# Performance work log

Measured on AMD Instinct MI355X. Metric: run time of the kernel, lower is better.

Reference implementation:

```python
import jax, jax.numpy as jnp
import numpy as np

EPS = 1e-5


def conv2d(x, w, b, pad, mode='reflect'):
    # x: [B,C,H,W], w: [O,I,kh,kw]
    if pad > 0:
        x = jnp.pad(x, ((0, 0), (0, 0), (pad, pad), (pad, pad)), mode=mode)
    y = jax.lax.conv_general_dilated(x, w, (1, 1), 'VALID',
                                     dimension_numbers=('NCHW', 'OIHW', 'NCHW'))
    return y + b[None, :, None, None]


def inorm(x):
    # InstanceNorm2d, no affine (nn.InstanceNorm2d default)
    m = jnp.mean(x, axis=(2, 3), keepdims=True)
    v = jnp.mean((x - m) ** 2, axis=(2, 3), keepdims=True)
    return (x - m) * jax.lax.rsqrt(v + EPS)


def upsample2(x):
    # nn.Upsample(scale_factor=2), default nearest
    return jnp.repeat(jnp.repeat(x, 2, axis=2), 2, axis=3)


def bilinear_sample(img, py, px):
    # img [B,C,H,W]; py/px [B,H,W] float coords; zero padding outside bounds
    B, C, H, W = img.shape
    y0 = jnp.floor(py)
    x0 = jnp.floor(px)
    wy1 = (py - y0)[:, None]
    wx1 = (px - x0)[:, None]
    wy0 = 1.0 - wy1
    wx0 = 1.0 - wx1
    y0i = y0.astype(jnp.int32)
    x0i = x0.astype(jnp.int32)
    flat = img.reshape(B, C, H * W)

    def tap(yi, xi):
        valid = (yi >= 0) & (yi < H) & (xi >= 0) & (xi < W)
        idx = jnp.clip(yi, 0, H - 1) * W + jnp.clip(xi, 0, W - 1)
        g = jnp.take_along_axis(flat, idx.reshape(B, 1, H * W), axis=2).reshape(B, C, H, W)
        return g * valid[:, None]

    return (tap(y0i, x0i) * wy0 * wx0 + tap(y0i, x0i + 1) * wy0 * wx1 +
            tap(y0i + 1, x0i) * wy1 * wx0 + tap(y0i + 1, x0i + 1) * wy1 * wx1)


def mdcn(x, offset, mask, w, b):
    # modulated deformable conv v2: 3x3, stride 1, pad 1, 1 deformable group
    # offset [B,18,H,W] read as interleaved (dy,dx) per kernel tap; mask [B,9,H,W]
    B, C, H, W = x.shape
    off = offset.reshape(B, 9, 2, H, W)
    base_y = jnp.arange(H, dtype=x.dtype)[None, :, None]
    base_x = jnp.arange(W, dtype=x.dtype)[None, None, :]
    cols = []
    for k in range(9):
        ky, kx = k // 3 - 1, k % 3 - 1
        py = base_y + ky + off[:, k, 0]
        px = base_x + kx + off[:, k, 1]
        cols.append(bilinear_sample(x, py, px) * mask[:, k][:, None])
    col = jnp.stack(cols, axis=2)  # [B,C,9,H,W]
    out = jnp.einsum('bckhw,ock->bohw', col, w.reshape(w.shape[0], C, 9))
    return out + b[None, :, None, None]


def dcn_block(out, skip, off_w, off_b, w, b):
    # ModulatedDeformConvPack(double=True): offsets from concat, deform conv on skip
    dc = jnp.concatenate([out, skip], axis=1)
    om = conv2d(dc, off_w, off_b, 1, mode='constant')
    o1, o2, m = jnp.split(om, 3, axis=1)
    offset = jnp.concatenate([o1, o2], axis=1)
    pre = mdcn(skip, offset, jax.nn.sigmoid(m), w, b)
    return jnp.concatenate([pre, out], axis=1), offset


def decoder_fwd(x, skip1, skip2,
                rb0_w1, rb0_b1, rb0_w2, rb0_b2,
                rb1_w1, rb1_b1, rb1_w2, rb1_b2,
                conv1_w, conv1_b, conv3_w, conv3_b,
                conv5_w, conv5_b, conv6_w, conv6_b,
                dcn2_off_w, dcn2_off_b, dcn2_w, dcn2_b,
                dcn1_off_w, dcn1_off_b, dcn1_w, dcn1_b):
    out = x
    # i=0: ResBlocks (2 resblocks, 'in' norm, relu, reflect pad)
    for (w1, b1, w2, b2) in ((rb0_w1, rb0_b1, rb0_w2, rb0_b2),
                             (rb1_w1, rb1_b1, rb1_w2, rb1_b2)):
        h = jax.nn.relu(inorm(conv2d(out, w1, b1, 1)))
        out = out + inorm(conv2d(h, w2, b2, 1))
    # i=1: Conv2dBlock(256->256, 5x5)
    out = jax.nn.relu(inorm(conv2d(out, conv1_w, conv1_b, 2)))
    # dcn_2 hook (baseline_idx=2 -> dcn_idx=[1,3])
    out, offset2 = dcn_block(out, skip2, dcn2_off_w, dcn2_off_b, dcn2_w, dcn2_b)
    # i=2: upsample
    out = upsample2(out)
    # i=3: Conv2dBlock(512->128, 5x5)
    out = jax.nn.relu(inorm(conv2d(out, conv3_w, conv3_b, 2)))
    # dcn hook
    out, offset1 = dcn_block(out, skip1, dcn1_off_w, dcn1_off_b, dcn1_w, dcn1_b)
    # i=4: upsample
    out = upsample2(out)
    # i=5: Conv2dBlock(256->64, 5x5)
    out = jax.nn.relu(inorm(conv2d(out, conv5_w, conv5_b, 2)))
    # i=6: Conv2dBlock(64->3, 7x7, no norm, tanh)
    out = jnp.tanh(conv2d(out, conv6_w, conv6_b, 3))
    offset_sum = 0.5 * (jnp.mean(jnp.abs(offset1)) + jnp.mean(jnp.abs(offset2)))
    return out, offset_sum


def setup_inputs() -> dict:
    key = jax.random.key(0)
    ks = iter(jax.random.split(key, 48))

    def randn(shape, scale=1.0):
        return jax.random.normal(next(ks), shape, dtype=jnp.float32) * scale

    def conv_w(o, i, k, scale=1.0):
        return randn((o, i, k, k), scale / float(np.sqrt(i * k * k)))

    d = {}
    d['x'] = randn((8, 256, 32, 32))
    d['skip1'] = randn((8, 128, 64, 64))
    d['skip2'] = randn((8, 256, 32, 32))
    for r in range(2):
        d[f'rb{r}_w1'] = conv_w(256, 256, 3)
        d[f'rb{r}_b1'] = randn((256,), 0.01)
        d[f'rb{r}_w2'] = conv_w(256, 256, 3)
        d[f'rb{r}_b2'] = randn((256,), 0.01)
    d['conv1_w'] = conv_w(256, 256, 5); d['conv1_b'] = randn((256,), 0.01)
    d['conv3_w'] = conv_w(128, 512, 5); d['conv3_b'] = randn((128,), 0.01)
    d['conv5_w'] = conv_w(64, 256, 5); d['conv5_b'] = randn((64,), 0.01)
    d['conv6_w'] = conv_w(3, 64, 7); d['conv6_b'] = randn((3,), 0.01)
    d['dcn2_off_w'] = conv_w(27, 512, 3, 0.1); d['dcn2_off_b'] = randn((27,), 0.01)
    d['dcn2_w'] = conv_w(256, 256, 3); d['dcn2_b'] = randn((256,), 0.01)
    d['dcn1_off_w'] = conv_w(27, 256, 3, 0.1); d['dcn1_off_b'] = randn((27,), 0.01)
    d['dcn1_w'] = conv_w(128, 128, 3); d['dcn1_b'] = randn((128,), 0.01)
    return d


def reference(x, skip1, skip2,
              rb0_w1, rb0_b1, rb0_w2, rb0_b2,
              rb1_w1, rb1_b1, rb1_w2, rb1_b2,
              conv1_w, conv1_b, conv3_w, conv3_b,
              conv5_w, conv5_b, conv6_w, conv6_b,
              dcn2_off_w, dcn2_off_b, dcn2_w, dcn2_b,
              dcn1_off_w, dcn1_off_b, dcn1_w, dcn1_b):
    return decoder_fwd(x, skip1, skip2,
                       rb0_w1, rb0_b1, rb0_w2, rb0_b2,
                       rb1_w1, rb1_b1, rb1_w2, rb1_b2,
                       conv1_w, conv1_b, conv3_w, conv3_b,
                       conv5_w, conv5_b, conv6_w, conv6_b,
                       dcn2_off_w, dcn2_off_b, dcn2_w, dcn2_b,
                       dcn1_off_w, dcn1_off_b, dcn1_w, dcn1_b)
```

## Files before the change

kernel.cpp:

```cpp
#include <hip/hip_runtime.h>
#include <hip/hip_bf16.h>
#include <math.h>

typedef __hip_bfloat16 bf16;
typedef unsigned short u16;
typedef __attribute__((ext_vector_type(8))) short short8;
typedef __attribute__((ext_vector_type(4))) float f32x4;

__device__ __forceinline__ float LD(const float* p) { return *p; }
__device__ __forceinline__ float LD(const bf16* p)  { return __bfloat162float(*p); }
__device__ __forceinline__ void  ST(float* p, float v) { *p = v; }
__device__ __forceinline__ void  ST(bf16* p, float v)  { *p = __float2bfloat16(v); }
__device__ __forceinline__ u16   f2b(float v) { bf16 h = __float2bfloat16(v); return *reinterpret_cast<u16*>(&h); }
__device__ __forceinline__ float b2fu(u16 u) { bf16 h = *reinterpret_cast<bf16*>(&u); return __bfloat162float(h); }

__global__ __launch_bounds__(256) void copy_kernel(const float* __restrict__ in,
                                                   float* __restrict__ out, int n) {
    int i = blockIdx.x * blockDim.x + threadIdx.x;
    if (i < n) out[i] = in[i];
}

__global__ __launch_bounds__(256) void nhwc_split_kernel(const float* __restrict__ in,
                                                         u16* __restrict__ hi, u16* __restrict__ lo,
                                                         int C, int HW)
{
    __shared__ float tile[32][65];
    const int b = blockIdx.z;
    const int c0 = blockIdx.y * 32;
    const int p0 = blockIdx.x * 64;
    for (int i = threadIdx.x; i < 2048; i += 256) {
        const int c_ = i >> 6, p_ = i & 63;
        tile[c_][p_] = in[((size_t)(b * C + c0 + c_)) * HW + p0 + p_];
    }
    __syncthreads();
    for (int i = threadIdx.x; i < 2048; i += 256) {
        const int p_ = i >> 5, c_ = i & 31;
        const float v = tile[c_][p_];
        const bf16 h = __float2bfloat16(v);
        const float hv = __bfloat162float(h);
        const bf16 l = __float2bfloat16(v - hv);
        const size_t dst = ((size_t)b * HW + p0 + p_) * C + c0 + c_;
        hi[dst] = *(const u16*)&h;
        lo[dst] = *(const u16*)&l;
    }
}

__global__ __launch_bounds__(256) void wsplit_kernel(const float* __restrict__ w,
                                                     u16* __restrict__ hi, u16* __restrict__ lo,
                                                     int O, int C, int KK)
{
    const int i = blockIdx.x * 256 + threadIdx.x;
    const int n = O * C * KK;
    if (i >= n) return;
    const int o = i / (C * KK);
    const int r = i - o * C * KK;
    const int c = r / KK;
    const int t = r - c * KK;
    const float v = w[i];
    const bf16 h = __float2bfloat16(v);
    const float hv = __bfloat162float(h);
    const bf16 l = __float2bfloat16(v - hv);
    const size_t dst = ((size_t)t * O + o) * C + c;
    hi[dst] = *(const u16*)&h;
    lo[dst] = *(const u16*)&l;
}

__global__ __launch_bounds__(256) void wsplit2_kernel(const float* __restrict__ w,
                                                      u16* __restrict__ hi, u16* __restrict__ lo,
                                                      int O, int C, int KK)
{
    const int i = blockIdx.x * 256 + threadIdx.x;
    const int n = O * C * KK;
    if (i >= n) return;
    const int o = i / (C * KK);
    const int r = i - o * C * KK;
    const int c = r / KK;
    const int t = r - c * KK;
    const float v = w[i];
    const bf16 h = __float2bfloat16(v);
    const float hv = __bfloat162float(h);
    const bf16 l = __float2bfloat16(v - hv);
    const int nch = C >> 5;
    const int cc = c >> 5, quad = (c >> 3) & 3, q = c & 7;
    const size_t dst = ((((size_t)t * nch + cc) * 4 + quad) * O + o) * 8 + q;
    hi[dst] = *(const u16*)&h;
    lo[dst] = *(const u16*)&l;
}

__global__ __launch_bounds__(256) void wsplitL_kernel(const float* __restrict__ w,
        u16* __restrict__ lh, u16* __restrict__ ll, u16* __restrict__ ch, int O, int C)
{
    const int i = blockIdx.x * 256 + threadIdx.x;
    const int n = O * C * 50;
    if (i >= n) return;
    const int s = i / (O * C);
    const int r = i - s * (O * C);
    const int o = r / C;
    const int c = r - o * C;
    const size_t U = (size_t)C * O;
    const int cc = c >> 5, quad = (c >> 3) & 3, q = c & 7;
    const size_t din = (((size_t)cc * 4 + quad) * O + o) * 8 + q;
    const float* wp = w + ((size_t)o * C + c) * 25;
    if (s < 30) {
        const int ry = s / 15, rem = s % 15, j = rem / 5, tx = rem % 5;
        int ys, yn;
        if (ry == 0) { ys = (j == 0) ? 0 : (j == 1) ? 2 : 4; yn = (j == 2) ? 1 : 2; }
        else         { ys = (j == 0) ? 0 : (j == 1) ? 1 : 3; yn = (j == 0) ? 1 : 2; }
        float v = 0.f;
        for (int ty = ys; ty < ys + yn; ++ty) v += wp[ty * 5 + tx];
        const bf16 h = __float2bfloat16(v);
        const bf16 l = __float2bfloat16(v - __bfloat162float(h));
        lh[(size_t)s * U + din] = *(const u16*)&h;
        ll[(size_t)s * U + din] = *(const u16*)&l;
    } else {
        const int t = s - 30;
        const int cidx = t / 5, tx = t - cidx * 5;
        const int tyc = (cidx == 0) ? 0 : (cidx == 1) ? 1 : (cidx == 2) ? 3 : 4;
        const bf16 h = __float2bfloat16(wp[tyc * 5 + tx]);
        ch[(size_t)t * U + din] = *(const u16*)&h;
    }
}

template<typename T1, typename T2, int K, bool UP, int EPI, bool ASPLIT,
         int NR, int NCOL, int MT, int MW>
__global__ __launch_bounds__(MW * 128) void conv_mfma3(
        const T1* __restrict__ src1, const T2* __restrict__ src2,
        int C1, int C,
        const u16* __restrict__ wth, const u16* __restrict__ wtl,
        const float* __restrict__ bias,
        void* __restrict__ outv, int O, int H, int W)
{
    constexpr int KK = K * K;
    constexpr int ATILE = NR * NCOL * 32;
    __shared__ __align__(16) u16 Ah[ATILE];
    __shared__ __align__(16) u16 Al[ASPLIT ? ATILE : 8];

    const int tid  = threadIdx.x;
    const int lane = tid & 63;
    const int wv   = tid >> 6;
    const int ln15 = lane & 15;
    const int quad = lane >> 4;
    const int mi = wv % MW, ni = wv / MW;
    const int b = blockIdx.y;
    const int p0 = blockIdx.x * (MT * 16 * MW);
    const int obase = blockIdx.z * 64;
    const int HW = H * W;
    const int SH = UP ? (H >> 1) : H;
    const int SW = UP ? (W >> 1) : W;
    const int SHW = SH * SW;
    const int PAD = K / 2;
    const int C2 = C - C1;
    const int nch = C >> 5;

    const int y0 = p0 / W;
    const int rbase = (y0 <= PAD) ? 0 : (UP ? ((y0 - PAD) >> 1) : (y0 - PAD));

    int rs[MT][K], cs[MT][K];
#pragma unroll
    for (int ms = 0; ms < MT; ++ms) {
        const int pm = p0 + mi * (MT * 16) + ms * 16 + ln15;
        const int ym = pm / W, xm = pm - ym * W;
#pragma unroll
        for (int tt = 0; tt < K; ++tt) {
            int yy = ym + tt - PAD;
            yy = yy < 0 ? -yy : yy; yy = yy >= H ? 2 * H - 2 - yy : yy;
            rs[ms][tt] = (UP ? (yy >> 1) : yy) - rbase;
            int xx = xm + tt - PAD;
            xx = xx < 0 ? -xx : xx; xx = xx >= W ? 2 * W - 2 - xx : xx;
            cs[ms][tt] = UP ? (xx >> 1) : xx;
        }
    }

    f32x4 acc[MT][2];
#pragma unroll
    for (int i = 0; i < MT; ++i)
#pragma unroll
        for (int j = 0; j < 2; ++j) acc[i][j] = (f32x4)0.f;

    for (int cc = 0; cc < nch; ++cc) {
        const int c0 = cc << 5;
        __syncthreads();
        for (int idx = tid; idx < NR * NCOL * 4; idx += MW * 128) {
            const int c_ = idx % NCOL;
            const int r_ = (idx / NCOL) % NR;
            const int cq = idx / (NCOL * NR);
            int rr = rbase + r_; rr = rr >= SH ? SH - 1 : rr;
            const int sidx = rr * SW + c_;
            short8 vh, vl;
#pragma unroll
            for (int q = 0; q < 8; ++q) {
                const int c = c0 + cq * 8 + q;
                float v;
                if (c < C1) v = LD(src1 + (size_t)(b * C1 + c) * SHW + sidx);
                else        v = LD(src2 + (size_t)(b * C2 + (c - C1)) * SHW + sidx);
                const u16 hv = f2b(v);
                vh[q] = (short)hv;
                if (ASPLIT) vl[q] = (short)f2b(v - b2fu(hv));
            }
            *(short8*)&Ah[idx * 8] = vh;
            if (ASPLIT) *(short8*)&Al[idx * 8] = vl;
        }
        __syncthreads();

#pragma unroll
        for (int t = 0; t < KK; ++t) {
            const int ty = t / K, tx = t - ty * K;
            const size_t wb0 = ((((size_t)t * nch + cc) * 4 + quad) * O
                                + obase + ni * 32 + ln15) * 8;
            const short8 b0h = *(const short8*)(wth + wb0);
            const short8 b1h = *(const short8*)(wth + wb0 + 128);
            const short8 b0l = *(const short8*)(wtl + wb0);
            const short8 b1l = *(const short8*)(wtl + wb0 + 128);
#pragma unroll
            for (int ms = 0; ms < MT; ++ms) {
                const int ao = ((quad * NR + rs[ms][ty]) * NCOL + cs[ms][tx]) * 8;
                const short8 a = *(const short8*)&Ah[ao];
                acc[ms][0] = __builtin_amdgcn_mfma_f32_16x16x32_bf16(a, b0h, acc[ms][0], 0, 0, 0);
                acc[ms][0] = __builtin_amdgcn_mfma_f32_16x16x32_bf16(a, b0l, acc[ms][0], 0, 0, 0);
                acc[ms][1] = __builtin_amdgcn_mfma_f32_16x16x32_bf16(a, b1h, acc[ms][1], 0, 0, 0);
                acc[ms][1] = __builtin_amdgcn_mfma_f32_16x16x32_bf16(a, b1l, acc[ms][1], 0, 0, 0);
                if (ASPLIT) {
                    const short8 al = *(const short8*)&Al[ao];
                    acc[ms][0] = __builtin_amdgcn_mfma_f32_16x16x32_bf16(al, b0h, acc[ms][0], 0, 0, 0);
                    acc[ms][1] = __builtin_amdgcn_mfma_f32_16x16x32_bf16(al, b1h, acc[ms][1], 0, 0, 0);
                }
            }
        }
    }

#pragma unroll
    for (int ms = 0; ms < MT; ++ms) {
#pragma unroll
        for (int ns = 0; ns < 2; ++ns) {
            const int o = obase + ni * 32 + ns * 16 + ln15;
            const float bv = bias[o];
            const f32x4 av = acc[ms][ns];
#pragma unroll
            for (int r = 0; r < 4; ++r) {
                const int pp = p0 + mi * (MT * 16) + ms * 16 + (quad << 2) + r;
                const float v = av[r] + bv;
                const size_t oidx = ((size_t)(b * O + o)) * HW + pp;
                if (EPI == 0) ((float*)outv)[oidx] = v;
                else          ((bf16*)outv)[oidx] = __float2bfloat16(v);
            }
        }
    }
}

template<typename T1, typename T2, int NR, int NCOL, int MT, int MW>
__global__ __launch_bounds__(MW * 128) void conv_mfma5(
        const T1* __restrict__ src1, const T2* __restrict__ src2,
        int C1, int C,
        const u16* __restrict__ wLh, const u16* __restrict__ wLl,
        const u16* __restrict__ wCh,
        const float* __restrict__ bias,
        bf16* __restrict__ out, int O, int H, int W)
{
    constexpr int NRR = NR + 1;
    __shared__ __align__(16) u16 Ah[4 * NRR * NCOL * 8];

    const int tid  = threadIdx.x;
    const int lane = tid & 63;
    const int wv   = tid >> 6;
    const int ln15 = lane & 15;
    const int quad = lane >> 4;
    const int mi = wv % MW, ni = wv / MW;
    const int b = blockIdx.y;
    const int p0 = blockIdx.x * (MT * 16 * MW);
    const int obase = blockIdx.z * 64;
    const int HW = H * W;
    const int SH = H >> 1, SW = W >> 1;
    const int SHW = SH * SW;
    const int C2 = C - C1;
    const int nch = C >> 5;
    const size_t U = (size_t)C * O;

    const int y0 = p0 / W;
    const int rbase = (y0 <= 2) ? 0 : ((y0 - 2) >> 1);

    const int ym0 = (p0 + mi * (MT * 16)) / W;
    const int ry = ym0 & 1;
    const int uu = ym0 >> 1;
    int r0 = uu - 1, r2 = uu + 1;
    r0 = r0 < 0 ? 1 : r0;
    r2 = r2 >= SH ? SH - 2 : r2;
    const int rg0 = r0 - rbase, rg1 = uu - rbase, rg2 = r2 - rbase;

    const bool isTopW = (ym0 <= 1), isBotW = (ym0 >= H - 2);
    const bool isBorderW = isTopW || isBotW;
    int cidx = 0;
    if (isTopW) cidx = (ym0 == 0) ? 1 : 0;
    if (isBotW) cidx = (ym0 == H - 2) ? 3 : 2;
    const bool blkTop = (p0 == 0);
    const bool blkBot = (p0 + MW * MT * 16 == HW);
    const bool blkEdge = blkTop || blkBot;

    int cs[MT][5];
#pragma unroll
    for (int ms = 0; ms < MT; ++ms) {
        const int pm = p0 + mi * (MT * 16) + ms * 16 + ln15;
        const int xm = pm % W;
#pragma unroll
        for (int tt = 0; tt < 5; ++tt) {
            int xx = xm + tt - 2;
            xx = xx < 0 ? -xx : xx; xx = xx >= W ? 2 * W - 2 - xx : xx;
            cs[ms][tt] = xx >> 1;
        }
    }

    f32x4 acc[MT][2];
#pragma unroll
    for (int i = 0; i < MT; ++i)
#pragma unroll
        for (int j = 0; j < 2; ++j) acc[i][j] = (f32x4)0.f;

    for (int cc = 0; cc < nch; ++cc) {
        const int c0 = cc << 5;
        __syncthreads();
        for (int idx = tid; idx < NR * NCOL * 4; idx += MW * 128) {
            const int c_ = idx % NCOL;
            const int r_ = (idx / NCOL) % NR;
            const int cq = idx / (NCOL * NR);
            int rr = rbase + r_; rr = rr >= SH ? SH - 1 : rr;
            const int sidx = rr * SW + c_;
            short8 vh;
#pragma unroll
            for (int q = 0; q < 8; ++q) {
                const int c = c0 + cq * 8 + q;
                float v;
                if (c < C1) v = LD(src1 + (size_t)(b * C1 + c) * SHW + sidx);
                else        v = LD(src2 + (size_t)(b * C2 + (c - C1)) * SHW + sidx);
                vh[q] = (short)f2b(v);
            }
            *(short8*)&Ah[((cq * NRR + r_) * NCOL + c_) * 8] = vh;
        }
        if (blkEdge) {
            const int ra = blkTop ? 0 : SH - 1;
            const int rb2 = blkTop ? 1 : SH - 2;
            for (int idx = tid; idx < NCOL * 4; idx += MW * 128) {
                const int c_ = idx % NCOL;
                const int cq = idx / NCOL;
                short8 vh;
#pragma unroll
                for (int q = 0; q < 8; ++q) {
                    const int c = c0 + cq * 8 + q;
                    float va, vb;
                    if (c < C1) {
                        const size_t base = (size_t)(b * C1 + c) * SHW;
                        va = LD(src1 + base + ra * SW + c_);
                        vb = LD(src1 + base + rb2 * SW + c_);
                    } else {
                        const size_t base = (size_t)(b * C2 + (c - C1)) * SHW;
                        va = LD(src2 + base + ra * SW + c_);
                        vb = LD(src2 + base + rb2 * SW + c_);
                    }
                    vh[q] = (short)f2b(va - vb);
                }
                *(short8*)&Ah[((cq * NRR + NR) * NCOL + c_) * 8] = vh;
            }
        }
        __syncthreads();

        const size_t wq = ((size_t)(cc * 4 + quad) * O + obase + ni * 32 + ln15) * 8;
#pragma unroll
        for (int j = 0; j < 3; ++j) {
            const int rgj = (j == 0) ? rg0 : (j == 1) ? rg1 : rg2;
#pragma unroll
            for (int tx = 0; tx < 5; ++tx) {
                const size_t wb = (size_t)((ry * 3 + j) * 5 + tx) * U + wq;
                const short8 b0h = *(const short8*)(wLh + wb);
                const short8 b1h = *(const short8*)(wLh + wb + 128);
                const short8 b0l = *(const short8*)(wLl + wb);
                const short8 b1l = *(const short8*)(wLl + wb + 128);
#pragma unroll
                for (int ms = 0; ms < MT; ++ms) {
                    const int ao = ((quad * NRR + rgj) * NCOL + cs[ms][tx]) * 8;
                    const short8 a = *(const short8*)&Ah[ao];
                    acc[ms][0] = __builtin_amdgcn_mfma_f32_16x16x32_bf16(a, b0h, acc[ms][0], 0, 0, 0);
                    acc[ms][0] = __builtin_amdgcn_mfma_f32_16x16x32_bf16(a, b0l, acc[ms][0], 0, 0, 0);
                    acc[ms][1] = __builtin_amdgcn_mfma_f32_16x16x32_bf16(a, b1h, acc[ms][1], 0, 0, 0);
                    acc[ms][1] = __builtin_amdgcn_mfma_f32_16x16x32_bf16(a, b1l, acc[ms][1], 0, 0, 0);
                }
            }
        }
        if (isBorderW) {
#pragma unroll
            for (int tx = 0; tx < 5; ++tx) {
                const size_t wb = (size_t)(cidx * 5 + tx) * U + wq;
                const short8 b0 = *(const short8*)(wCh + wb);
                const short8 b1 = *(const short8*)(wCh + wb + 128);
#pragma unroll
                for (int ms = 0; ms < MT; ++ms) {
                    const int ao = ((quad * NRR + NR) * NCOL + cs[ms][tx]) * 8;
                    const short8 a = *(const short8*)&Ah[ao];
                    acc[ms][0] = __builtin_amdgcn_mfma_f32_16x16x32_bf16(a, b0, acc[ms][0], 0, 0, 0);
                    acc[ms][1] = __builtin_amdgcn_mfma_f32_16x16x32_bf16(a, b1, acc[ms][1], 0, 0, 0);
                }
            }
        }
    }

#pragma unroll
    for (int ms = 0; ms < MT; ++ms) {
#pragma unroll
        for (int ns = 0; ns < 2; ++ns) {
            const int o = obase + ni * 32 + ns * 16 + ln15;
            const float bv = bias[o];
            const f32x4 av = acc[ms][ns];
#pragma unroll
            for (int r = 0; r < 4; ++r) {
                const int pp = p0 + mi * (MT * 16) + ms * 16 + (quad << 2) + r;
                out[((size_t)(b * O + o)) * HW + pp] = __float2bfloat16(av[r] + bv);
            }
        }
    }
}

template<typename OT, bool ASPLIT>
__global__ __launch_bounds__(256) void mdcn_mfma(
        const u16* __restrict__ skiph, const u16* __restrict__ skipl,
        const float* __restrict__ om,
        const u16* __restrict__ wth, const u16* __restrict__ wtl,
        const float* __restrict__ bias,
        OT* __restrict__ out, int C, int O, int H, int W)
{
    __shared__ float tpy[576], tpxs[576], tms[576];
    __shared__ __align__(16) u16 Ah[2][2048];
    __shared__ __align__(16) u16 Al[ASPLIT ? 2 : 1][2048];
    __shared__ __align__(16) u16 Bs[2][2][2048];

    const int tid = threadIdx.x;
    const int lane = tid & 63;
    const int wv = tid >> 6;
    const int ln15 = lane & 15;
    const int quad = lane >> 4;
    const int mi = wv & 1, ni = wv >> 1;
    const int flat = blockIdx.x + gridDim.x * (blockIdx.y + 8 * blockIdx.z);
    const int b = flat & 7;
    const int rest = flat >> 3;
    const int p0 = (rest % gridDim.x) * 64;
    const int obase = (rest / gridDim.x) * 64;
    const int HW = H * W;
    const int nch = C >> 5;

    const float* omb = om + (size_t)b * 27 * HW;
    for (int i = tid; i < 576; i += 256) {
        const int k = i >> 6, px_ = i & 63;
        const int p = p0 + px_;
        const int y = p / W, x = p - y * W;
        const float dy = omb[(2 * k) * HW + p];
        const float dx = omb[(2 * k + 1) * HW + p];
        const float mk = 1.f / (1.f + expf(-omb[(18 + k) * HW + p]));
        float py = (float)(y + k / 3 - 1) + dy;
        float pxx = (float)(x + k % 3 - 1) + dx;
        py  = fminf(fmaxf(py, -2.f), (float)H + 1.f);
        pxx = fminf(fmaxf(pxx, -2.f), (float)W + 1.f);
        tpy[i] = py; tpxs[i] = pxx; tms[i] = mk;
    }
    __syncthreads();

    f32x4 acc[2][2];
#pragma unroll
    for (int i = 0; i < 2; ++i)
#pragma unroll
        for (int j = 0; j < 2; ++j) acc[i][j] = (f32x4)0.f;

    const u16* xbh = skiph + (size_t)b * HW * C;
    const u16* xbl = skipl + (size_t)b * HW * C;
    const int swA = (lane >> 1) & 3;
    const int awr = (lane * 4 + (wv ^ swA)) * 8;
    const int pix0 = mi * 32 + ln15;
    const int pix1 = pix0 + 16;
    const int ao0 = (pix0 * 4 + (quad ^ ((pix0 >> 1) & 3))) * 8;
    const int ao1 = (pix1 * 4 + (quad ^ ((pix1 >> 1) & 3))) * 8;
    const int bo0 = (quad * 64 + ni * 32 + ln15) * 8;
    const int bo1 = bo0 + 16 * 8;

    int chunk = 0;
    for (int cc = 0; cc < nch; ++cc) {
        const int cbase = (cc << 5) + (wv << 3);
        for (int k = 0; k < 9; ++k, ++chunk) {
            const int s = chunk & 1;
            const float py = tpy[k * 64 + lane], pxx = tpxs[k * 64 + lane], mk = tms[k * 64 + lane];
            const float y0f = floorf(py), x0f = floorf(pxx);
            const int y0 = (int)y0f, x0 = (int)x0f;
            const float wy1 = py - y0f, wx1 = pxx - x0f;
            const float wy0 = 1.f - wy1, wx0 = 1.f - wx1;
            const bool r0v = (y0 >= 0 && y0 < H), r1v = (y0 + 1 >= 0 && y0 + 1 < H);
            const bool c0v = (x0 >= 0 && x0 < W), c1v = (x0 + 1 >= 0 && x0 + 1 < W);
            const float w00 = (r0v && c0v) ? wy0 * wx0 * mk : 0.f;
            const float w01 = (r0v && c1v) ? wy0 * wx1 * mk : 0.f;
            const float w10 = (r1v && c0v) ? wy1 * wx0 * mk : 0.f;
            const float w11 = (r1v && c1v) ? wy1 * wx1 * mk : 0.f;
            const int i00 = (r0v ? y0 : 0) * W + (c0v ? x0 : 0);
            const int i01 = (r0v ? y0 : 0) * W + (c1v ? x0 + 1 : 0);
            const int i10 = (r1v ? y0 + 1 : 0) * W + (c0v ? x0 : 0);
            const int i11 = (r1v ? y0 + 1 : 0) * W + (c1v ? x0 + 1 : 0);
            {
                const short8 h00 = *(const short8*)(xbh + (size_t)i00 * C + cbase);
                const short8 h01 = *(const short8*)(xbh + (size_t)i01 * C + cbase);
                const short8 h10 = *(const short8*)(xbh + (size_t)i10 * C + cbase);
                const short8 h11 = *(const short8*)(xbh + (size_t)i11 * C + cbase);
                const short8 l00 = *(const short8*)(xbl + (size_t)i00 * C + cbase);
                const short8 l01 = *(const short8*)(xbl + (size_t)i01 * C + cbase);
                const short8 l10 = *(const short8*)(xbl + (size_t)i10 * C + cbase);
                const short8 l11 = *(const short8*)(xbl + (size_t)i11 * C + cbase);
                short8 vh, vl;
#pragma unroll
                for (int q = 0; q < 8; ++q) {
                    const float x00 = b2fu((u16)h00[q]) + b2fu((u16)l00[q]);
                    const float x01 = b2fu((u16)h01[q]) + b2fu((u16)l01[q]);
                    const float x10 = b2fu((u16)h10[q]) + b2fu((u16)l10[q]);
                    const float x11 = b2fu((u16)h11[q]) + b2fu((u16)l11[q]);
                    const float v = w00 * x00 + w01 * x01 + w10 * x10 + w11 * x11;
                    const u16 hv = f2b(v);
                    vh[q] = (short)hv;
                    if (ASPLIT) vl[q] = (short)f2b(v - b2fu(hv));
                }
                *(short8*)&Ah[s][awr] = vh;
                if (ASPLIT) *(short8*)&Al[s][awr] = vl;
            }
            {
                const size_t base = ((((size_t)k * nch + cc) * 4 + wv) * O + obase + lane) * 8;
                *(short8*)&Bs[s][0][tid * 8] = *(const short8*)(wth + base);
                *(short8*)&Bs[s][1][tid * 8] = *(const short8*)(wtl + base);
            }
            __syncthreads();
            const short8 a0 = *(const short8*)&Ah[s][ao0];
            const short8 a1 = *(const short8*)&Ah[s][ao1];
            const short8 b0h = *(const short8*)&Bs[s][0][bo0];
            const short8 b1h = *(const short8*)&Bs[s][0][bo1];
            const short8 b0l = *(const short8*)&Bs[s][1][bo0];
            const short8 b1l = *(const short8*)&Bs[s][1][bo1];
            acc[0][0] = __builtin_amdgcn_mfma_f32_16x16x32_bf16(a0, b0h, acc[0][0], 0, 0, 0);
            acc[0][0] = __builtin_amdgcn_mfma_f32_16x16x32_bf16(a0, b0l, acc[0][0], 0, 0, 0);
            acc[0][1] = __builtin_amdgcn_mfma_f32_16x16x32_bf16(a0, b1h, acc[0][1], 0, 0, 0);
            acc[0][1] = __builtin_amdgcn_mfma_f32_16x16x32_bf16(a0, b1l, acc[0][1], 0, 0, 0);
            acc[1][0] = __builtin_amdgcn_mfma_f32_16x16x32_bf16(a1, b0h, acc[1][0], 0, 0, 0);
            acc[1][0] = __builtin_amdgcn_mfma_f32_16x16x32_bf16(a1, b0l, acc[1][0], 0, 0, 0);
            acc[1][1] = __builtin_amdgcn_mfma_f32_16x16x32_bf16(a1, b1h, acc[1][1], 0, 0, 0);
            acc[1][1] = __builtin_amdgcn_mfma_f32_16x16x32_bf16(a1, b1l, acc[1][1], 0, 0, 0);
            if (ASPLIT) {
                const short8 a0l = *(const short8*)&Al[s][ao0];
                const short8 a1l = *(const short8*)&Al[s][ao1];
                acc[0][0] = __builtin_amdgcn_mfma_f32_16x16x32_bf16(a0l, b0h, acc[0][0], 0, 0, 0);
                acc[0][1] = __builtin_amdgcn_mfma_f32_16x16x32_bf16(a0l, b1h, acc[0][1], 0, 0, 0);
                acc[1][0] = __builtin_amdgcn_mfma_f32_16x16x32_bf16(a1l, b0h, acc[1][0], 0, 0, 0);
                acc[1][1] = __builtin_amdgcn_mfma_f32_16x16x32_bf16(a1l, b1h, acc[1][1], 0, 0, 0);
            }
        }
    }

#pragma unroll
    for (int ms = 0; ms < 2; ++ms) {
#pragma unroll
        for (int ns = 0; ns < 2; ++ns) {
            const int o = obase + ni * 32 + ns * 16 + ln15;
            const float bv = bias[o];
#pragma unroll
            for (int r = 0; r < 4; ++r) {
                const int pp = p0 + mi * 32 + ms * 16 + (quad << 2) + r;
                ST(out + ((size_t)(b * O + o)) * HW + pp, acc[ms][ns][r] + bv);
            }
        }
    }
}

template<typename T1, typename T2, int K, bool REFLECT, bool UP, int NTN, int EPI, bool ASPLIT>
__global__ __launch_bounds__(256) void conv_mfma(
        const T1* __restrict__ src1, const T2* __restrict__ src2,
        int C1, int C,
        const u16* __restrict__ wth, const u16* __restrict__ wtl,
        const float* __restrict__ bias,
        void* __restrict__ outv, int O, int H, int W)
{
    constexpr int KK = K * K;
    __shared__ __align__(16) u16 As[64 * 40];
    __shared__ __align__(16) u16 Alo[ASPLIT ? 64 * 40 : 8];
    __shared__ __align__(16) u16 Bh[NTN * 16 * 40];
    __shared__ __align__(16) u16 Bl[NTN * 16 * 40];

    const int tid  = threadIdx.x;
    const int wv   = tid >> 6;
    const int lane = tid & 63;
    const int ln15 = lane & 15;
    const int flat = blockIdx.x + gridDim.x * blockIdx.y;
    const int b    = flat & 7;
    const int p0   = (flat >> 3) * 64;
    const int obase = blockIdx.z * (NTN * 16);
    const int HW = H * W;
    const int Hs = UP ? (H >> 1) : H;
    const int Ws = UP ? (W >> 1) : W;
    const int HsWs = Hs * Ws;
    const int PAD = K / 2;
    const int C2 = C - C1;
    const int m_stage = tid & 63;

    const int p = p0 + m_stage;
    const int y = p / W, x = p - y * W;
    int off[KK];
    float msk[KK];
#pragma unroll
    for (int ty = 0; ty < K; ++ty) {
#pragma unroll
        for (int tx = 0; tx < K; ++tx) {
            int yy = y + ty - PAD, xx = x + tx - PAD;
            bool vv = true;
            if (REFLECT) {
                yy = yy < 0 ? -yy : yy; yy = yy >= H ? 2 * H - 2 - yy : yy;
                xx = xx < 0 ? -xx : xx; xx = xx >= W ? 2 * W - 2 - xx : xx;
            } else {
                vv = (yy >= 0 && yy < H && xx >= 0 && xx < W);
                yy = yy < 0 ? 0 : (yy >= H ? H - 1 : yy);
                xx = xx < 0 ? 0 : (xx >= W ? W - 1 : xx);
            }
            off[ty * K + tx] = (UP ? (yy >> 1) : yy) * Ws + (UP ? (xx >> 1) : xx);
            msk[ty * K + tx] = vv ? 1.f : 0.f;
        }
    }

    f32x4 acc[NTN];
#pragma unroll
    for (int nt = 0; nt < NTN; ++nt) acc[nt] = (f32x4)0.f;

    const int aswz = (m_stage >> 3) & 3;
    const int awr  = m_stage * 40 + ((wv ^ aswz) << 3);
    const int arow = wv * 16 + ln15;
    const int ard  = arow * 40 + (((lane >> 4) ^ ((arow >> 3) & 3)) << 3);

    const int nch = C >> 5;
    for (int cc = 0; cc < nch; ++cc) {
        const int c0 = cc << 5;
        for (int t = 0; t < KK; ++t) {
            const int offt = off[t];
            const float mskt = msk[t];
            __syncthreads();
            {
                short8 avh, avl;
#pragma unroll
                for (int q = 0; q < 8; ++q) {
                    const int c = c0 + (wv << 3) + q;
                    float v;
                    if (c < C1) v = LD(src1 + ((size_t)(b * C1 + c)) * HsWs + offt);
                    else        v = LD(src2 + ((size_t)(b * C2 + (c - C1))) * HsWs + offt);
                    if (!REFLECT) v *= mskt;
                    const u16 hv = f2b(v);
                    avh[q] = (short)hv;
                    if (ASPLIT) avl[q] = (short)f2b(v - b2fu(hv));
                }
                *(short8*)&As[awr] = avh;
                if (ASPLIT) *(short8*)&Alo[awr] = avl;
            }
            for (int i = tid; i < NTN * 16 * 4; i += 256) {
                const int row = i >> 2, part = i & 3;
                int o = obase + row; if (o >= O) o = O - 1;
                const int pw = row * 40 + ((part ^ ((row >> 3) & 3)) << 3);
                const size_t wb = ((size_t)t * O + o) * C + c0 + (part << 3);
                *(short8*)&Bh[pw] = *(const short8*)(wth + wb);
                *(short8*)&Bl[pw] = *(const short8*)(wtl + wb);
            }
            __syncthreads();
            const short8 a = *(const short8*)&As[ard];
            short8 al;
            if (ASPLIT) al = *(const short8*)&Alo[ard];
#pragma unroll
            for (int nt = 0; nt < NTN; ++nt) {
                const int brow = nt * 16 + ln15;
                const int brd = brow * 40 + (((lane >> 4) ^ ((brow >> 3) & 3)) << 3);
                const short8 bh = *(const short8*)&Bh[brd];
                acc[nt] = __builtin_amdgcn_mfma_f32_16x16x32_bf16(a, bh, acc[nt], 0, 0, 0);
                const short8 bl = *(const short8*)&Bl[brd];
                acc[nt] = __builtin_amdgcn_mfma_f32_16x16x32_bf16(a, bl, acc[nt], 0, 0, 0);
                if (ASPLIT)
                    acc[nt] = __builtin_amdgcn_mfma_f32_16x16x32_bf16(al, bh, acc[nt], 0, 0, 0);
            }
        }
    }

#pragma unroll
    for (int nt = 0; nt < NTN; ++nt) {
        const int o = obase + nt * 16 + ln15;
        if (o < O) {
            const float bv = bias[o];
#pragma unroll
            for (int r = 0; r < 4; ++r) {
                const int pp = p0 + wv * 16 + ((lane >> 4) << 2) + r;
                const float v = acc[nt][r] + bv;
                const size_t oidx = ((size_t)(b * O + o)) * HW + pp;
                if (EPI == 0)      ((float*)outv)[oidx] = v;
                else if (EPI == 1) ((float*)outv)[oidx] = tanhf(v);
                else               ((bf16*)outv)[oidx] = __float2bfloat16(v);
            }
        }
    }
}

template<typename T>
__global__ __launch_bounds__(256) void inorm_kernel(T* __restrict__ buf,
                                                    float* __restrict__ resid,
                                                    int HW, int mode)
{
    __shared__ double sh0[256], sh1[256];
    const int pl = blockIdx.x;
    T* p = buf + (size_t)pl * HW;
    double s = 0.0, ss = 0.0;
    for (int i = threadIdx.x; i < HW; i += 256) {
        float v = LD(p + i);
        s += (double)v; ss += (double)v * (double)v;
    }
    sh0[threadIdx.x] = s; sh1[threadIdx.x] = ss;
    __syncthreads();
    for (int st = 128; st > 0; st >>= 1) {
        if (threadIdx.x < st) {
            sh0[threadIdx.x] += sh0[threadIdx.x + st];
            sh1[threadIdx.x] += sh1[threadIdx.x + st];
        }
        __syncthreads();
    }
    const double mean = sh0[0] / HW;
    const float m = (float)mean;
    const float var = (float)(sh1[0] / HW - mean * mean);
    const float inv = rsqrtf(var + 1e-5f);
    if (mode == 0) {
        for (int i = threadIdx.x; i < HW; i += 256) {
            float v = (LD(p + i) - m) * inv;
            ST(p + i, v > 0.f ? v : 0.f);
        }
    } else {
        float* r = resid + (size_t)pl * HW;
        for (int i = threadIdx.x; i < HW; i += 256)
            r[i] = r[i] + (LD(p + i) - m) * inv;
    }
}

__global__ void zero1_kernel(float* __restrict__ out) { if (threadIdx.x == 0) out[0] = 0.f; }

__global__ __launch_bounds__(256) void offsum_one(const float* __restrict__ om, int HW,
                                                  float* __restrict__ out)
{
    __shared__ double sh[256];
    const int n = 8 * 18 * HW;
    double s = 0.0;
    for (int i = blockIdx.x * 256 + threadIdx.x; i < n; i += gridDim.x * 256) {
        const int b = i / (18 * HW); const int r = i - b * 18 * HW;
        const int c = r / HW; const int p = r - c * HW;
        s += fabs((double)om[(size_t)(b * 27 + c) * HW + p]);
    }
    sh[threadIdx.x] = s;
    __syncthreads();
    for (int st = 128; st > 0; st >>= 1) {
        if (threadIdx.x < st) sh[threadIdx.x] += sh[threadIdx.x + st];
        __syncthreads();
    }
    if (threadIdx.x == 0) atomicAdd(out, (float)(0.5 * sh[0] / n));
}

extern "C" void kernel_launch(void* const* d_in, const int* in_sizes, int n_in,
                              void* d_out, int out_size, void* d_ws, size_t ws_size,
                              hipStream_t stream)
{
    if (n_in < 27) return;
    if (out_size < 393217) return;
    if (in_sizes[0] != 8 * 256 * 32 * 32) return;
    if (in_sizes[1] != 8 * 128 * 64 * 64) return;
    if (in_sizes[2] != 8 * 256 * 32 * 32) return;
    if (in_sizes[25] != 128 * 128 * 9) return;
    if (in_sizes[26] != 128) return;

    const float* x        = (const float*)d_in[0];
    const float* skip1    = (const float*)d_in[1];
    const float* skip2    = (const float*)d_in[2];
    const float* rbw[2][2] = {{(const float*)d_in[3], (const float*)d_in[5]},
                              {(const float*)d_in[7], (const float*)d_in[9]}};
    const float* rbb[2][2] = {{(const float*)d_in[4], (const float*)d_in[6]},
                              {(const float*)d_in[8], (const float*)d_in[10]}};
    const float* conv1_w = (const float*)d_in[11]; const float* conv1_b = (const float*)d_in[12];
    const float* conv3_w = (const float*)d_in[13]; const float* conv3_b = (const float*)d_in[14];
    const float* conv5_w = (const float*)d_in[15]; const float* conv5_b = (const float*)d_in[16];
    const float* conv6_w = (const float*)d_in[17]; const float* conv6_b = (const float*)d_in[18];
    const float* dcn2_off_w = (const float*)d_in[19]; const float* dcn2_off_b = (const float*)d_in[20];
    const float* dcn2_w = (const float*)d_in[21]; const float* dcn2_b = (const float*)d_in[22];
    const float* dcn1_off_w = (const float*)d_in[23]; const float* dcn1_off_b = (const float*)d_in[24];
    const float* dcn1_w = (const float*)d_in[25]; const float* dcn1_b = (const float*)d_in[26];

    float* outp = (float*)d_out;

    const size_t NEED_F32 = 9494528ull;
    if (ws_size < NEED_F32 * 4ull) return;

    float* ws = (float*)d_ws;
    const size_t NA = 2097152ull;
    float* A   = ws;
    float* Bb  = ws + NA;
    float* Tmp = ws + 2 * NA;
    float* om2 = ws + 3 * NA;
    float* om1 = om2 + 221184;
    bf16*  Fb  = (bf16*)(om1 + 884736);
    bf16*  Ib  = (bf16*)A;
    bf16*  Jb  = (bf16*)Bb;
    u16*   wm2h = (u16*)Tmp;
    u16*   wm2l = wm2h + 589824;
    u16*   wo2h = (u16*)(Tmp + 589824);
    u16*   wo2l = wo2h + 124416;
    u16*   wL3h = (u16*)Tmp;
    u16*   wL3l = wL3h + 30 * 65536;
    u16*   wC3h = wL3l + 30 * 65536;
    u16*   wm1h = (u16*)om2;
    u16*   wm1l = wm1h + 147456;
    u16*   wo1h = wm1h + 294912;
    u16*   wo1l = wo1h + 62208;
    u16*   wL5h = (u16*)om1;
    u16*   wL5l = wL5h + 30 * 16384;
    u16*   wC5h = wL5l + 30 * 16384;
    u16*   wt6h = (u16*)om2;
    u16*   wt6l = wt6h + 9408;
    u16*   wEh = (u16*)Fb;
    u16*   s2h = (u16*)Fb;
    u16*   s2l = s2h + 2097152;
    u16*   s1h = (u16*)Bb;
    u16*   s1l = (u16*)Tmp;

    copy_kernel<<<8192, 256, 0, stream>>>(x, A, (int)NA);

    for (int r = 0; r < 2; ++r) {
        wsplit2_kernel<<<2304, 256, 0, stream>>>(rbw[r][0], wEh, wEh + 589824, 256, 256, 9);
        conv_mfma3<float, float, 3, false, 0, true, 4, 32, 2, 2><<<dim3(16, 8, 4), 256, 0, stream>>>(
            A, (const float*)nullptr, 256, 256, wEh, wEh + 589824, rbb[r][0], Bb, 256, 32, 32);
        inorm_kernel<float><<<2048, 256, 0, stream>>>(Bb, nullptr, 1024, 0);
        wsplit2_kernel<<<2304, 256, 0, stream>>>(rbw[r][1], wEh, wEh + 589824, 256, 256, 9);
        conv_mfma3<float, float, 3, false, 0, true, 4, 32, 2, 2><<<dim3(16, 8, 4), 256, 0, stream>>>(
            Bb, (const float*)nullptr, 256, 256, wEh, wEh + 589824, rbb[r][1], Tmp, 256, 32, 32);
        inorm_kernel<float><<<2048, 256, 0, stream>>>(Tmp, A, 1024, 1);
    }

    wsplit2_kernel<<<6400, 256, 0, stream>>>(conv1_w, wEh, wEh + 1638400, 256, 256, 25);
    conv_mfma3<float, float, 5, false, 0, true, 6, 32, 2, 2><<<dim3(16, 8, 4), 256, 0, stream>>>(
        A, (const float*)nullptr, 256, 256, wEh, wEh + 1638400, conv1_b, Bb, 256, 32, 32);
    inorm_kernel<float><<<2048, 256, 0, stream>>>(Bb, nullptr, 1024, 0);

    nhwc_split_kernel<<<dim3(16, 8, 8), 256, 0, stream>>>(skip2, s2h, s2l, 256, 1024);

    wsplit_kernel<<<486, 256, 0, stream>>>(dcn2_off_w, wo2h, wo2l, 27, 512, 9);
    conv_mfma<float, float, 3, false, false, 2, 0, false><<<dim3(16, 8, 1), 256, 0, stream>>>(
        Bb, skip2, 256, 512, wo2h, wo2l, dcn2_off_b, om2, 27, 32, 32);
    wsplit2_kernel<<<2304, 256, 0, stream>>>(dcn2_w, wm2h, wm2l, 256, 256, 9);
    mdcn_mfma<float, true><<<dim3(16, 8, 4), 256, 0, stream>>>(
        s2h, s2l, om2, wm2h, wm2l, dcn2_b, A, 256, 256, 32, 32);

    zero1_kernel<<<1, 64, 0, stream>>>(outp + 393216);
    offsum_one<<<64, 256, 0, stream>>>(om2, 1024, outp + 393216);

    wsplitL_kernel<<<12800, 256, 0, stream>>>(conv3_w, wL3h, wL3l, wC3h, 128, 512);
    conv_mfma5<float, float, 4, 32, 4, 4><<<dim3(16, 8, 2), 512, 0, stream>>>(
        A, Bb, 256, 512, wL3h, wL3l, wC3h, conv3_b, Fb, 128, 64, 64);
    inorm_kernel<bf16><<<1024, 256, 0, stream>>>(Fb, nullptr, 4096, 0);

    wsplit_kernel<<<243, 256, 0, stream>>>(dcn1_off_w, wo1h, wo1l, 27, 256, 9);
    conv_mfma<bf16, float, 3, false, false, 2, 0, false><<<dim3(64, 8, 1), 256, 0, stream>>>(
        Fb, skip1, 128, 256, wo1h, wo1l, dcn1_off_b, om1, 27, 64, 64);
    wsplit2_kernel<<<576, 256, 0, stream>>>(dcn1_w, wm1h, wm1l, 128, 128, 9);
    nhwc_split_kernel<<<dim3(64, 4, 8), 256, 0, stream>>>(skip1, s1h, s1l, 128, 4096);
    mdcn_mfma<bf16, true><<<dim3(64, 8, 2), 256, 0, stream>>>(
        s1h, s1l, om1, wm1h, wm1l, dcn1_b, Ib, 128, 128, 64, 64);

    offsum_one<<<64, 256, 0, stream>>>(om1, 4096, outp + 393216);

    wsplitL_kernel<<<3200, 256, 0, stream>>>(conv5_w, wL5h, wL5l, wC5h, 64, 256);
    conv_mfma5<bf16, bf16, 3, 64, 4, 4><<<dim3(64, 8, 1), 512, 0, stream>>>(
        Ib, Fb, 128, 256, wL5h, wL5l, wC5h, conv5_b, Jb, 64, 128, 128);
    inorm_kernel<bf16><<<512, 256, 0, stream>>>(Jb, nullptr, 16384, 0);

    wsplit_kernel<<<37, 256, 0, stream>>>(conv6_w, wt6h, wt6l, 3, 64, 49);
    conv_mfma<bf16, float, 7, true, false, 1, 1, false><<<dim3(256, 8, 1), 256, 0, stream>>>(
        Jb, (const float*)nullptr, 64, 64, wt6h, wt6l, conv6_b, (void*)outp, 3, 128, 128);
}
```

Baseline: 1.439 ms.

## Gather deformable-conv samples from fp32 NHWC input and hoist tap math out of channel loop

The skip tensors are now transposed to fp32 NHWC instead of being split into bf16 hi/lo pairs, so the deformable-conv kernel gathers fp32 values with 16-byte vector loads. This removes the per-element hi+lo reconstruction. The loop order is swapped so the kernel tap is outermost, and the bilinear coordinates, weights and indices are computed once per tap rather than once per channel chunk. The gathered bytes per sample stay the same (fp32 versus two bf16), but the changed loop order alters the temporal locality of the gathers across channel chunks.

```diff
diff --git a/kernel.cpp b/kernel.cpp
--- a/kernel.cpp
+++ b/kernel.cpp
@@ -20,9 +20,9 @@
     if (i < n) out[i] = in[i];
 }
 
-__global__ __launch_bounds__(256) void nhwc_split_kernel(const float* __restrict__ in,
-                                                         u16* __restrict__ hi, u16* __restrict__ lo,
-                                                         int C, int HW)
+__global__ __launch_bounds__(256) void nhwc_f32_kernel(const float* __restrict__ in,
+                                                       float* __restrict__ out,
+                                                       int C, int HW)
 {
     __shared__ float tile[32][65];
     const int b = blockIdx.z;
@@ -35,13 +35,7 @@
     __syncthreads();
     for (int i = threadIdx.x; i < 2048; i += 256) {
         const int p_ = i >> 5, c_ = i & 31;
-        const float v = tile[c_][p_];
-        const bf16 h = __float2bfloat16(v);
-        const float hv = __bfloat162float(h);
-        const bf16 l = __float2bfloat16(v - hv);
-        const size_t dst = ((size_t)b * HW + p0 + p_) * C + c0 + c_;
-        hi[dst] = *(const u16*)&h;
-        lo[dst] = *(const u16*)&l;
+        out[((size_t)b * HW + p0 + p_) * C + c0 + c_] = tile[c_][p_];
     }
 }
 
@@ -418,7 +412,7 @@
 
 template<typename OT, bool ASPLIT>
 __global__ __launch_bounds__(256) void mdcn_mfma(
-        const u16* __restrict__ skiph, const u16* __restrict__ skipl,
+        const float* __restrict__ skipf,
         const float* __restrict__ om,
         const u16* __restrict__ wth, const u16* __restrict__ wtl,
         const float* __restrict__ bias,
@@ -465,8 +459,7 @@
 #pragma unroll
         for (int j = 0; j < 2; ++j) acc[i][j] = (f32x4)0.f;
 
-    const u16* xbh = skiph + (size_t)b * HW * C;
-    const u16* xbl = skipl + (size_t)b * HW * C;
+    const float* xb = skipf + (size_t)b * HW * C;
     const int swA = (lane >> 1) & 3;
     const int awr = (lane * 4 + (wv ^ swA)) * 8;
     const int pix0 = mi * 32 + ln15;
@@ -477,45 +470,52 @@
     const int bo1 = bo0 + 16 * 8;
 
     int chunk = 0;
-    for (int cc = 0; cc < nch; ++cc) {
-        const int cbase = (cc << 5) + (wv << 3);
-        for (int k = 0; k < 9; ++k, ++chunk) {
+    for (int k = 0; k < 9; ++k) {
+        const float py = tpy[k * 64 + lane], pxx = tpxs[k * 64 + lane], mk = tms[k * 64 + lane];
+        const float y0f = floorf(py), x0f = floorf(pxx);
+        const int y0 = (int)y0f, x0 = (int)x0f;
+        const float wy1 = py - y0f, wx1 = pxx - x0f;
+        const float wy0 = 1.f - wy1, wx0 = 1.f - wx1;
+        const bool r0v = (y0 >= 0 && y0 < H), r1v = (y0 + 1 >= 0 && y0 + 1 < H);
+        const bool c0v = (x0 >= 0 && x0 < W), c1v = (x0 + 1 >= 0 && x0 + 1 < W);
+        const float w00 = (r0v && c0v) ? wy0 * wx0 * mk : 0.f;
+        const float w01 = (r0v && c1v) ? wy0 * wx1 * mk : 0.f;
+        const float w10 = (r1v && c0v) ? wy1 * wx0 * mk : 0.f;
+        const float w11 = (r1v && c1v) ? wy1 * wx1 * mk : 0.f;
+        const int i00 = (r0v ? y0 : 0) * W + (c0v ? x0 : 0);
+        const int i01 = (r0v ? y0 : 0) * W + (c1v ? x0 + 1 : 0);
+        const int i10 = (r1v ? y0 + 1 : 0) * W + (c0v ? x0 : 0);
+        const int i11 = (r1v ? y0 + 1 : 0) * W + (c1v ? x0 + 1 : 0);
+        const float* pt00 = xb + (size_t)i00 * C;
+        const float* pt01 = xb + (size_t)i01 * C;
+        const float* pt10 = xb + (size_t)i10 * C;
+        const float* pt11 = xb + (size_t)i11 * C;
+        for (int cc = 0; cc < nch; ++cc, ++chunk) {
             const int s = chunk & 1;
-            const float py = tpy[k * 64 + lane], pxx = tpxs[k * 64 + lane], mk = tms[k * 64 + lane];
-            const float y0f = floorf(py), x0f = floorf(pxx);
-            const int y0 = (int)y0f, x0 = (int)x0f;
-            const float wy1 = py - y0f, wx1 = pxx - x0f;
-            const float wy0 = 1.f - wy1, wx0 = 1.f - wx1;
-            const bool r0v = (y0 >= 0 && y0 < H), r1v = (y0 + 1 >= 0 && y0 + 1 < H);
-            const bool c0v = (x0 >= 0 && x0 < W), c1v = (x0 + 1 >= 0 && x0 + 1 < W);
-            const float w00 = (r0v && c0v) ? wy0 * wx0 * mk : 0.f;
-            const float w01 = (r0v && c1v) ? wy0 * wx1 * mk : 0.f;
-            const float w10 = (r1v && c0v) ? wy1 * wx0 * mk : 0.f;
-            const float w11 = (r1v && c1v) ? wy1 * wx1 * mk : 0.f;
-            const int i00 = (r0v ? y0 : 0) * W + (c0v ? x0 : 0);
-            const int i01 = (r0v ? y0 : 0) * W + (c1v ? x0 + 1 : 0);
-            const int i10 = (r1v ? y0 + 1 : 0) * W + (c0v ? x0 : 0);
-            const int i11 = (r1v ? y0 + 1 : 0) * W + (c1v ? x0 + 1 : 0);
+            const int cbase = (cc << 5) + (wv << 3);
             {
-                const short8 h00 = *(const short8*)(xbh + (size_t)i00 * C + cbase);
-                const short8 h01 = *(const short8*)(xbh + (size_t)i01 * C + cbase);
-                const short8 h10 = *(const short8*)(xbh + (size_t)i10 * C + cbase);
-                const short8 h11 = *(const short8*)(xbh + (size_t)i11 * C + cbase);
-                const short8 l00 = *(const short8*)(xbl + (size_t)i00 * C + cbase);
-                const short8 l01 = *(const short8*)(xbl + (size_t)i01 * C + cbase);
-                const short8 l10 = *(const short8*)(xbl + (size_t)i10 * C + cbase);
-                const short8 l11 = *(const short8*)(xbl + (size_t)i11 * C + cbase);
+                const f32x4 a00 = *(const f32x4*)(pt00 + cbase);
+                const f32x4 b00 = *(const f32x4*)(pt00 + cbase + 4);
+                const f32x4 a01 = *(const f32x4*)(pt01 + cbase);
+                const f32x4 b01 = *(const f32x4*)(pt01 + cbase + 4);
+                const f32x4 a10 = *(const f32x4*)(pt10 + cbase);
+                const f32x4 b10 = *(const f32x4*)(pt10 + cbase + 4);
+                const f32x4 a11 = *(const f32x4*)(pt11 + cbase);
+                const f32x4 b11 = *(const f32x4*)(pt11 + cbase + 4);
                 short8 vh, vl;
 #pragma unroll
-                for (int q = 0; q < 8; ++q) {
-                    const float x00 = b2fu((u16)h00[q]) + b2fu((u16)l00[q]);
-                    const float x01 = b2fu((u16)h01[q]) + b2fu((u16)l01[q]);
-                    const float x10 = b2fu((u16)h10[q]) + b2fu((u16)l10[q]);
-                    const float x11 = b2fu((u16)h11[q]) + b2fu((u16)l11[q]);
-                    const float v = w00 * x00 + w01 * x01 + w10 * x10 + w11 * x11;
+                for (int q = 0; q < 4; ++q) {
+                    const float v = w00 * a00[q] + w01 * a01[q] + w10 * a10[q] + w11 * a11[q];
                     const u16 hv = f2b(v);
                     vh[q] = (short)hv;
                     if (ASPLIT) vl[q] = (short)f2b(v - b2fu(hv));
+                }
+#pragma unroll
+                for (int q = 0; q < 4; ++q) {
+                    const float v = w00 * b00[q] + w01 * b01[q] + w10 * b10[q] + w11 * b11[q];
+                    const u16 hv = f2b(v);
+                    vh[4 + q] = (short)hv;
+                    if (ASPLIT) vl[4 + q] = (short)f2b(v - b2fu(hv));
                 }
                 *(short8*)&Ah[s][awr] = vh;
                 if (ASPLIT) *(short8*)&Al[s][awr] = vl;
@@ -815,10 +815,8 @@
     u16*   wt6h = (u16*)om2;
     u16*   wt6l = wt6h + 9408;
     u16*   wEh = (u16*)Fb;
-    u16*   s2h = (u16*)Fb;
-    u16*   s2l = s2h + 2097152;
-    u16*   s1h = (u16*)Bb;
-    u16*   s1l = (u16*)Tmp;
+    float* s2f = (float*)Fb;
+    float* s1f = Bb;
 
     copy_kernel<<<8192, 256, 0, stream>>>(x, A, (int)NA);
 
@@ -838,14 +836,14 @@
         A, (const float*)nullptr, 256, 256, wEh, wEh + 1638400, conv1_b, Bb, 256, 32, 32);
     inorm_kernel<float><<<2048, 256, 0, stream>>>(Bb, nullptr, 1024, 0);
 
-    nhwc_split_kernel<<<dim3(16, 8, 8), 256, 0, stream>>>(skip2, s2h, s2l, 256, 1024);
+    nhwc_f32_kernel<<<dim3(16, 8, 8), 256, 0, stream>>>(skip2, s2f, 256, 1024);
 
     wsplit_kernel<<<486, 256, 0, stream>>>(dcn2_off_w, wo2h, wo2l, 27, 512, 9);
     conv_mfma<float, float, 3, false, false, 2, 0, false><<<dim3(16, 8, 1), 256, 0, stream>>>(
         Bb, skip2, 256, 512, wo2h, wo2l, dcn2_off_b, om2, 27, 32, 32);
     wsplit2_kernel<<<2304, 256, 0, stream>>>(dcn2_w, wm2h, wm2l, 256, 256, 9);
     mdcn_mfma<float, true><<<dim3(16, 8, 4), 256, 0, stream>>>(
-        s2h, s2l, om2, wm2h, wm2l, dcn2_b, A, 256, 256, 32, 32);
+        s2f, om2, wm2h, wm2l, dcn2_b, A, 256, 256, 32, 32);
 
     zero1_kernel<<<1, 64, 0, stream>>>(outp + 393216);
     offsum_one<<<64, 256, 0, stream>>>(om2, 1024, outp + 393216);
@@ -859,9 +857,9 @@
     conv_mfma<bf16, float, 3, false, false, 2, 0, false><<<dim3(64, 8, 1), 256, 0, stream>>>(
         Fb, skip1, 128, 256, wo1h, wo1l, dcn1_off_b, om1, 27, 64, 64);
     wsplit2_kernel<<<576, 256, 0, stream>>>(dcn1_w, wm1h, wm1l, 128, 128, 9);
-    nhwc_split_kernel<<<dim3(64, 4, 8), 256, 0, stream>>>(skip1, s1h, s1l, 128, 4096);
+    nhwc_f32_kernel<<<dim3(64, 4, 8), 256, 0, stream>>>(skip1, s1f, 128, 4096);
     mdcn_mfma<bf16, true><<<dim3(64, 8, 2), 256, 0, stream>>>(
-        s1h, s1l, om1, wm1h, wm1l, dcn1_b, Ib, 128, 128, 64, 64);
+        s1f, om1, wm1h, wm1l, dcn1_b, Ib, 128, 128, 64, 64);
 
     offsum_one<<<64, 256, 0, stream>>>(om1, 4096, outp + 393216);
 
```

After: 1.432 ms. No clear change (-0.5%).
